# Performance work log

Hardware: AMD Instinct MI355X
Metric: run time of the kernel (lower is better)

The kernel has to match this reference:

```python
import jax, jax.numpy as jnp
import numpy as np

# cv2.getGaussianKernel(5, 0) returns the fixed small-kernel table [1,4,6,4,1]/16
_K5 = jnp.array([1.0, 4.0, 6.0, 4.0, 1.0], dtype=jnp.float32) / 16.0


def _blur5(x):
    """Separable 5x5 Gaussian blur with BORDER_REFLECT_101 (cv2 default). x: (..., H, W)."""
    H, W = x.shape[-2], x.shape[-1]
    pad = [(0, 0)] * (x.ndim - 2) + [(2, 2), (2, 2)]
    xp = jnp.pad(x, pad, mode='reflect')  # reflect == REFLECT_101
    xh = sum(_K5[i] * xp[..., i:i + H, :] for i in range(5))      # conv along H
    return sum(_K5[j] * xh[..., :, j:j + W] for j in range(5))    # conv along W


def _erode(m):
    # skimage binary_erosion: cross footprint, out-of-image treated as True
    p = [(0, 0)] * (m.ndim - 2) + [(1, 1), (1, 1)]
    mp = jnp.pad(m, p, constant_values=True)
    return (mp[..., 1:-1, 1:-1] & mp[..., :-2, 1:-1] & mp[..., 2:, 1:-1]
            & mp[..., 1:-1, :-2] & mp[..., 1:-1, 2:])


def _dilate(m):
    # skimage binary_dilation: cross footprint, out-of-image treated as False
    p = [(0, 0)] * (m.ndim - 2) + [(1, 1), (1, 1)]
    mp = jnp.pad(m, p, constant_values=False)
    return (mp[..., 1:-1, 1:-1] | mp[..., :-2, 1:-1] | mp[..., 2:, 1:-1]
            | mp[..., 1:-1, :-2] | mp[..., 1:-1, 2:])


def _fill_holes(m):
    """remove_small_holes with area_threshold > H*W == fill every enclosed hole.
    Background = flood fill of ~m seeded from the image border (4-connectivity)."""
    comp = ~m
    H, W = m.shape[-2], m.shape[-1]
    border = jnp.zeros((H, W), bool)
    border = border.at[0, :].set(True).at[-1, :].set(True)
    border = border.at[:, 0].set(True).at[:, -1].set(True)
    seed = comp & border

    def cond(st):
        return st[1]

    def body(st):
        s, _ = st
        ns = comp & _dilate(s)
        return ns, jnp.any(ns != s)

    bg, _ = jax.lax.while_loop(cond, body, (seed, jnp.array(True)))
    return ~bg  # foreground plus all enclosed holes


def _get_mask(img, maxv, th):
    """clip -> uint8 quantize -> 5x5 Gaussian blur -> threshold -> opening -> hole fill."""
    norm = jnp.clip(img, 0.0, maxv) / maxv            # min_=0, max_=img.max()
    q = jnp.floor(255.0 * norm)                        # np.uint8 cast truncates
    b = jnp.round(_blur5(q))                           # cv2 uint8 blur rounds to nearest
    m = b > th
    m = _dilate(_erode(m))                             # binary opening, cross footprint
    return _fill_holes(m)


def setup_inputs() -> dict:
    key = jax.random.key(0)
    x = jax.random.normal(key, (16, 37, 224, 224), dtype=jnp.float32)
    return {"input": x, "label": 1}


def reference(input, label):
    if label:
        lab = jnp.argmax(input, axis=1).astype(jnp.float32)            # (B, H, W)
        maxv = lab.max(axis=(-2, -1), keepdims=True)
        m = _get_mask(lab, maxv, 0.0)
        out = jnp.repeat(m[:, None], 3, axis=1)                        # (B, 3, H, W)
    else:
        x = (input + 1.0) / 2.0
        maxv = x.max(axis=(-3, -2, -1), keepdims=True)
        m = _get_mask(x, maxv, 55.0)
        out = m
    return out.astype(jnp.float32)
```

## Files before the change

kernel.cpp:

```cpp
#include <hip/hip_runtime.h>
#include <stdint.h>

#define NB 16
#define NC 37
#define H 224
#define W 224
#define HW (H * W)
#define WPR 7
#define IMG_WORDS (H * WPR)
#define QUADS_PER_IMG (HW / 4)
#define BLOCKS_PER_IMG (QUADS_PER_IMG / 256)

__global__ __launch_bounds__(256) void k_argmax(const float* __restrict__ in,
                                                uint8_t* __restrict__ lab,
                                                int* __restrict__ bmax) {
    const int b = blockIdx.x / BLOCKS_PER_IMG;
    const int qid = blockIdx.x * 256 + threadIdx.x;
    const int p = (qid % QUADS_PER_IMG) * 4;
    const float4* base = (const float4*)(in + (size_t)b * NC * HW + p);
    float4 bv = base[0];
    int ix = 0, iy = 0, iz = 0, iw = 0;
#pragma unroll
    for (int c = 1; c < NC; c += 4) {
        float4 a0 = base[(size_t)(c + 0) * (HW / 4)];
        float4 a1 = base[(size_t)(c + 1) * (HW / 4)];
        float4 a2 = base[(size_t)(c + 2) * (HW / 4)];
        float4 a3 = base[(size_t)(c + 3) * (HW / 4)];
        if (a0.x > bv.x) { bv.x = a0.x; ix = c; }
        if (a0.y > bv.y) { bv.y = a0.y; iy = c; }
        if (a0.z > bv.z) { bv.z = a0.z; iz = c; }
        if (a0.w > bv.w) { bv.w = a0.w; iw = c; }
        if (a1.x > bv.x) { bv.x = a1.x; ix = c + 1; }
        if (a1.y > bv.y) { bv.y = a1.y; iy = c + 1; }
        if (a1.z > bv.z) { bv.z = a1.z; iz = c + 1; }
        if (a1.w > bv.w) { bv.w = a1.w; iw = c + 1; }
        if (a2.x > bv.x) { bv.x = a2.x; ix = c + 2; }
        if (a2.y > bv.y) { bv.y = a2.y; iy = c + 2; }
        if (a2.z > bv.z) { bv.z = a2.z; iz = c + 2; }
        if (a2.w > bv.w) { bv.w = a2.w; iw = c + 2; }
        if (a3.x > bv.x) { bv.x = a3.x; ix = c + 3; }
        if (a3.y > bv.y) { bv.y = a3.y; iy = c + 3; }
        if (a3.z > bv.z) { bv.z = a3.z; iz = c + 3; }
        if (a3.w > bv.w) { bv.w = a3.w; iw = c + 3; }
    }
    uint32_t packed = (uint32_t)ix | ((uint32_t)iy << 8) |
                      ((uint32_t)iz << 16) | ((uint32_t)iw << 24);
    *(uint32_t*)(lab + (size_t)b * HW + p) = packed;

    int mymax = max(max(ix, iy), max(iz, iw));
    __shared__ int smax;
    if (threadIdx.x == 0) smax = 0;
    __syncthreads();
    atomicMax(&smax, mymax);
    __syncthreads();
    if (threadIdx.x == 0) bmax[blockIdx.x] = smax;
}

__global__ __launch_bounds__(256) void k_mask(const uint8_t* __restrict__ lab,
                                              const int* __restrict__ bmax,
                                              uint32_t* __restrict__ mbits) {
    __shared__ int qlut[NC];
    __shared__ int smax;
    const int tid = threadIdx.x;
    const int b = blockIdx.x / BLOCKS_PER_IMG;
    if (tid == 0) smax = 0;
    __syncthreads();
    if (tid < BLOCKS_PER_IMG) atomicMax(&smax, bmax[b * BLOCKS_PER_IMG + tid]);
    __syncthreads();
    if (tid < NC) {
        int mv = smax;
        qlut[tid] = (mv > 0) ? (int)floorf(255.0f * ((float)tid / (float)mv)) : 0;
    }
    __syncthreads();

    const int qid = blockIdx.x * 256 + tid;
    const int rem = qid % QUADS_PER_IMG;
    const int h = rem / (W / 4);
    const int w0 = (rem % (W / 4)) * 4;
    const uint8_t* __restrict__ L = lab + (size_t)b * HW;

    int S0 = 0, S1 = 0, S2 = 0, S3 = 0;
    const int kw5[5] = {1, 4, 6, 4, 1};
#pragma unroll
    for (int i = 0; i < 5; ++i) {
        int r = h + i - 2;
        r = (r < 0) ? -r : ((r > H - 1) ? (2 * (H - 1) - r) : r);
        const uint8_t* row = L + r * W;
        int q0, q1, q2, q3, q4, q5, q6, q7;
        if (w0 >= 4 && w0 <= W - 8) {
            uint32_t wa = *(const uint32_t*)(row + w0 - 4);
            uint32_t wb = *(const uint32_t*)(row + w0);
            uint32_t wc = *(const uint32_t*)(row + w0 + 4);
            q0 = qlut[(wa >> 16) & 0xff];
            q1 = qlut[(wa >> 24) & 0xff];
            q2 = qlut[wb & 0xff];
            q3 = qlut[(wb >> 8) & 0xff];
            q4 = qlut[(wb >> 16) & 0xff];
            q5 = qlut[(wb >> 24) & 0xff];
            q6 = qlut[wc & 0xff];
            q7 = qlut[(wc >> 8) & 0xff];
        } else {
            int qq[8];
#pragma unroll
            for (int t = 0; t < 8; ++t) {
                int c2 = w0 - 2 + t;
                c2 = (c2 < 0) ? -c2 : ((c2 > W - 1) ? (2 * (W - 1) - c2) : c2);
                qq[t] = qlut[row[c2]];
            }
            q0 = qq[0]; q1 = qq[1]; q2 = qq[2]; q3 = qq[3];
            q4 = qq[4]; q5 = qq[5]; q6 = qq[6]; q7 = qq[7];
        }
        int sh0 = q0 + 4 * q1 + 6 * q2 + 4 * q3 + q4;
        int sh1 = q1 + 4 * q2 + 6 * q3 + 4 * q4 + q5;
        int sh2 = q2 + 4 * q3 + 6 * q4 + 4 * q5 + q6;
        int sh3 = q3 + 4 * q4 + 6 * q5 + 4 * q6 + q7;
        int k = kw5[i];
        S0 += k * sh0; S1 += k * sh1; S2 += k * sh2; S3 += k * sh3;
    }
    uint32_t nib = (S0 > 128 ? 1u : 0u) | (S1 > 128 ? 2u : 0u) |
                   (S2 > 128 ? 4u : 0u) | (S3 > 128 ? 8u : 0u);
    uint32_t wword = nib << ((tid & 7) * 4);
    wword |= __shfl_xor(wword, 1);
    wword |= __shfl_xor(wword, 2);
    wword |= __shfl_xor(wword, 4);
    if ((tid & 7) == 0) mbits[qid >> 3] = wword;
}

__global__ __launch_bounds__(256) void k_fill(const uint32_t* __restrict__ mbits,
                                              uint32_t* __restrict__ fg) {
    const int b = blockIdx.x;
    const int tid = threadIdx.x;
    __shared__ uint32_t A[IMG_WORDS];
    __shared__ uint32_t Bw[IMG_WORDS];
    __shared__ int s_changed;

    const uint32_t* src = mbits + b * IMG_WORDS;
    for (int i = tid; i < IMG_WORDS; i += 256) A[i] = src[i];
    __syncthreads();

    for (int i = tid; i < IMG_WORDS; i += 256) {
        int h = i / WPR, k = i % WPR;
        uint32_t cur = A[i];
        uint32_t north = (h > 0) ? A[i - WPR] : 0xFFFFFFFFu;
        uint32_t south = (h < H - 1) ? A[i + WPR] : 0xFFFFFFFFu;
        uint32_t west = (cur << 1) | ((k > 0) ? (A[i - 1] >> 31) : 1u);
        uint32_t east = (cur >> 1) | ((k < WPR - 1) ? (A[i + 1] << 31) : 0x80000000u);
        Bw[i] = cur & north & south & west & east;
    }
    __syncthreads();
    for (int i = tid; i < IMG_WORDS; i += 256) {
        int h = i / WPR, k = i % WPR;
        uint32_t cur = Bw[i];
        uint32_t north = (h > 0) ? Bw[i - WPR] : 0u;
        uint32_t south = (h < H - 1) ? Bw[i + WPR] : 0u;
        uint32_t west = (cur << 1) | ((k > 0) ? (Bw[i - 1] >> 31) : 0u);
        uint32_t east = (cur >> 1) | ((k < WPR - 1) ? (Bw[i + 1] << 31) : 0u);
        A[i] = cur | north | south | west | east;
    }
    __syncthreads();
    for (int i = tid; i < IMG_WORDS; i += 256) {
        int h = i / WPR, k = i % WPR;
        uint32_t comp = ~A[i];
        uint32_t border = (h == 0 || h == H - 1)
                              ? 0xFFFFFFFFu
                              : (((k == 0) ? 1u : 0u) | ((k == WPR - 1) ? 0x80000000u : 0u));
        Bw[i] = comp & border;
    }
    __syncthreads();

    while (true) {
        if (tid == 0) s_changed = 0;
        __syncthreads();
        if (tid < WPR) {
            const int k = tid;
            uint32_t carry = 0;
            for (int h = 0; h < H; ++h) {
                int i = h * WPR + k;
                uint32_t comp = ~A[i];
                uint32_t s = Bw[i];
                uint32_t ns = comp & (s | carry);
                if (ns != s) { Bw[i] = ns; s_changed = 1; }
                carry = ns;
            }
            carry = 0;
            for (int h = H - 1; h >= 0; --h) {
                int i = h * WPR + k;
                uint32_t comp = ~A[i];
                uint32_t s = Bw[i];
                uint32_t ns = comp & (s | carry);
                if (ns != s) { Bw[i] = ns; s_changed = 1; }
                carry = ns;
            }
        }
        __syncthreads();
        if (tid < H) {
            const int base = tid * WPR;
            uint32_t carry = 0;
            for (int k = 0; k < WPR; ++k) {
                uint32_t comp = ~A[base + k];
                uint32_t s = Bw[base + k];
                if (comp == 0u) { carry = 0u; continue; }
                uint32_t f = s | (carry & comp);
                uint32_t m = comp;
                f |= m & (f << 1);  m &= (m << 1);
                f |= m & (f << 2);  m &= (m << 2);
                f |= m & (f << 4);  m &= (m << 4);
                f |= m & (f << 8);  m &= (m << 8);
                f |= m & (f << 16);
                carry = f >> 31;
                if (f != s) { Bw[base + k] = f; s_changed = 1; }
            }
            carry = 0;
            for (int k = WPR - 1; k >= 0; --k) {
                uint32_t comp = ~A[base + k];
                uint32_t s = Bw[base + k];
                if (comp == 0u) { carry = 0u; continue; }
                uint32_t f = s | ((carry << 31) & comp);
                uint32_t m = comp;
                f |= m & (f >> 1);  m &= (m >> 1);
                f |= m & (f >> 2);  m &= (m >> 2);
                f |= m & (f >> 4);  m &= (m >> 4);
                f |= m & (f >> 8);  m &= (m >> 8);
                f |= m & (f >> 16);
                carry = f & 1u;
                if (f != s) { Bw[base + k] = f; s_changed = 1; }
            }
        }
        __syncthreads();
        int done = (s_changed == 0);
        __syncthreads();
        if (done) break;
    }

    uint32_t* dst = fg + b * IMG_WORDS;
    for (int i = tid; i < IMG_WORDS; i += 256) dst[i] = ~Bw[i];
}

__global__ __launch_bounds__(256) void k_expand(const uint32_t* __restrict__ fg,
                                                float* __restrict__ out) {
    const int qid = blockIdx.x * 256 + threadIdx.x;
    if (qid >= NB * 3 * H * (W / 4)) return;
    const int wq = qid % (W / 4);
    const int t = qid / (W / 4);
    const int h = t % H;
    const int b = (t / H) / 3;
    uint32_t word = fg[b * IMG_WORDS + h * WPR + (wq >> 3)];
    const int sh = (wq & 7) * 4;
    float4 v;
    v.x = ((word >> sh) & 1u) ? 1.0f : 0.0f;
    v.y = ((word >> (sh + 1)) & 1u) ? 1.0f : 0.0f;
    v.z = ((word >> (sh + 2)) & 1u) ? 1.0f : 0.0f;
    v.w = ((word >> (sh + 3)) & 1u) ? 1.0f : 0.0f;
    ((float4*)out)[qid] = v;
}

extern "C" void kernel_launch(void* const* d_in, const int* in_sizes, int n_in,
                              void* d_out, int out_size, void* d_ws, size_t ws_size,
                              hipStream_t stream) {
    const float* in = (const float*)d_in[0];
    float* out = (float*)d_out;

    uint8_t* lab = (uint8_t*)d_ws;
    int* bmax = (int*)((char*)d_ws + 802816);
    uint32_t* mbits = (uint32_t*)((char*)d_ws + 806400);
    uint32_t* fgb = (uint32_t*)((char*)d_ws + 906752);

    k_argmax<<<NB * BLOCKS_PER_IMG, 256, 0, stream>>>(in, lab, bmax);
    k_mask<<<NB * BLOCKS_PER_IMG, 256, 0, stream>>>(lab, bmax, mbits);
    k_fill<<<NB, 256, 0, stream>>>(mbits, fgb);
    k_expand<<<(NB * 3 * H * (W / 4) + 255) / 256, 256, 0, stream>>>(fgb, out);
}
```

Before: 218.5 us.

## Fuse hole-fill and output expansion, replicating fill across 16 blocks per image

Merges the flood-fill and float expansion kernels into one, launching 16 blocks per image. Each block redundantly recomputes the full opening and flood fill, then writes its 1/16 slice of the 3-channel float output straight from shared memory. This removes one kernel launch and the round trip of the foreground bitmap through global memory. It also spreads the output writes over more blocks than the old one-block-per-image fill, in exchange for 16x redundant fill computation.

```diff
diff --git a/kernel.cpp b/kernel.cpp
--- a/kernel.cpp
+++ b/kernel.cpp
@@ -10,6 +10,9 @@
 #define IMG_WORDS (H * WPR)
 #define QUADS_PER_IMG (HW / 4)
 #define BLOCKS_PER_IMG (QUADS_PER_IMG / 256)
+#define REPS 16
+#define OUT_Q4_PER_IMG (3 * H * (W / 4))
+#define OUT_Q4_PER_REP (OUT_Q4_PER_IMG / REPS)
 
 __global__ __launch_bounds__(256) void k_argmax(const float* __restrict__ in,
                                                 uint8_t* __restrict__ lab,
@@ -126,15 +129,16 @@
     if ((tid & 7) == 0) mbits[qid >> 3] = wword;
 }
 
-__global__ __launch_bounds__(256) void k_fill(const uint32_t* __restrict__ mbits,
-                                              uint32_t* __restrict__ fg) {
-    const int b = blockIdx.x;
+__global__ __launch_bounds__(256) void k_fillexp(const uint32_t* __restrict__ mbits,
+                                                 float* __restrict__ out) {
+    const int img = blockIdx.x >> 4;
+    const int rep = blockIdx.x & 15;
     const int tid = threadIdx.x;
     __shared__ uint32_t A[IMG_WORDS];
     __shared__ uint32_t Bw[IMG_WORDS];
     __shared__ int s_changed;
 
-    const uint32_t* src = mbits + b * IMG_WORDS;
+    const uint32_t* src = mbits + img * IMG_WORDS;
     for (int i = tid; i < IMG_WORDS; i += 256) A[i] = src[i];
     __syncthreads();
 
@@ -232,26 +236,21 @@
         if (done) break;
     }
 
-    uint32_t* dst = fg + b * IMG_WORDS;
-    for (int i = tid; i < IMG_WORDS; i += 256) dst[i] = ~Bw[i];
-}
-
-__global__ __launch_bounds__(256) void k_expand(const uint32_t* __restrict__ fg,
-                                                float* __restrict__ out) {
-    const int qid = blockIdx.x * 256 + threadIdx.x;
-    if (qid >= NB * 3 * H * (W / 4)) return;
-    const int wq = qid % (W / 4);
-    const int t = qid / (W / 4);
-    const int h = t % H;
-    const int b = (t / H) / 3;
-    uint32_t word = fg[b * IMG_WORDS + h * WPR + (wq >> 3)];
-    const int sh = (wq & 7) * 4;
-    float4 v;
-    v.x = ((word >> sh) & 1u) ? 1.0f : 0.0f;
-    v.y = ((word >> (sh + 1)) & 1u) ? 1.0f : 0.0f;
-    v.z = ((word >> (sh + 2)) & 1u) ? 1.0f : 0.0f;
-    v.w = ((word >> (sh + 3)) & 1u) ? 1.0f : 0.0f;
-    ((float4*)out)[qid] = v;
+    float4* outq = (float4*)out + (size_t)img * OUT_Q4_PER_IMG;
+    for (int oi = rep * OUT_Q4_PER_REP + tid; oi < (rep + 1) * OUT_Q4_PER_REP;
+         oi += 256) {
+        int remq = oi % QUADS_PER_IMG;
+        int h = remq / (W / 4);
+        int wq = remq % (W / 4);
+        uint32_t word = ~Bw[h * WPR + (wq >> 3)];
+        int sh = (wq & 7) * 4;
+        float4 v;
+        v.x = ((word >> sh) & 1u) ? 1.0f : 0.0f;
+        v.y = ((word >> (sh + 1)) & 1u) ? 1.0f : 0.0f;
+        v.z = ((word >> (sh + 2)) & 1u) ? 1.0f : 0.0f;
+        v.w = ((word >> (sh + 3)) & 1u) ? 1.0f : 0.0f;
+        outq[oi] = v;
+    }
 }
 
 extern "C" void kernel_launch(void* const* d_in, const int* in_sizes, int n_in,
@@ -263,10 +262,8 @@
     uint8_t* lab = (uint8_t*)d_ws;
     int* bmax = (int*)((char*)d_ws + 802816);
     uint32_t* mbits = (uint32_t*)((char*)d_ws + 806400);
-    uint32_t* fgb = (uint32_t*)((char*)d_ws + 906752);
 
     k_argmax<<<NB * BLOCKS_PER_IMG, 256, 0, stream>>>(in, lab, bmax);
     k_mask<<<NB * BLOCKS_PER_IMG, 256, 0, stream>>>(lab, bmax, mbits);
-    k_fill<<<NB, 256, 0, stream>>>(mbits, fgb);
-    k_expand<<<(NB * 3 * H * (W / 4) + 255) / 256, 256, 0, stream>>>(fgb, out);
-}
+    k_fillexp<<<NB * REPS, 256, 0, stream>>>(mbits, out);
+}
```

Measured after the change: 215.1 us. About the same (-1.6%).
